# Kernel tuning notes

Hardware: AMD Instinct MI355X
Metric: run time of the kernel (lower is better)

## Reference

```python
import math
import jax, jax.numpy as jnp
import numpy as np

B, TQ, TK = 16, 2048, 1024
D_DEC, D_ENC, D_ATT = 256, 256, 128
WINDOW_SIZE = 3


def setup_inputs() -> dict:
    key = jax.random.key(0)
    ks = jax.random.split(key, 11)
    s = 0.02
    return {
        "query": jax.random.normal(ks[0], (B, TQ, D_DEC), jnp.float32),
        "keys": jax.random.normal(ks[1], (B, TK, D_ENC), jnp.float32),
        "values": jax.random.normal(ks[2], (B, TK, D_ENC), jnp.float32),
        "Wq": jax.random.normal(ks[3], (D_ATT, D_DEC), jnp.float32) * s,
        "bq": jax.random.normal(ks[4], (D_ATT,), jnp.float32) * s,
        "Wk": jax.random.normal(ks[5], (D_ATT, D_ENC), jnp.float32) * s,
        "bk": jax.random.normal(ks[6], (D_ATT,), jnp.float32) * s,
        "Wv": jax.random.normal(ks[7], (D_ATT, D_ENC), jnp.float32) * s,
        "bv": jax.random.normal(ks[8], (D_ATT,), jnp.float32) * s,
        "Wo": jax.random.normal(ks[9], (D_DEC, D_ATT), jnp.float32) * s,
        "bo": jax.random.normal(ks[10], (D_DEC,), jnp.float32) * s,
        "prev_max_attention_idx": 100,
    }


def reference(query, keys, values, Wq, bq, Wk, bk, Wv, bv, Wo, bo,
              prev_max_attention_idx):
    residual = query
    q = query @ Wq.T + bq            # [B, Tq, A]
    k = keys @ Wk.T + bk             # [B, Tk, A]
    v = values @ Wv.T + bv           # [B, Tk, A]
    scores = jnp.einsum('bqa,bka->bqk', q, k)  # [B, Tq, Tk]
    Tk = scores.shape[-1]
    col = jnp.arange(Tk)
    # mask [:prev] if prev > 0, and [prev + window :] if in range
    masked = (col < prev_max_attention_idx) | (col >= prev_max_attention_idx + WINDOW_SIZE)
    scores = jnp.where(masked[None, None, :], -jnp.inf, scores)
    attn = jax.nn.softmax(scores, axis=-1)
    attn_scores = attn
    # dropout_prob = 0.0 -> identity
    ctx = jnp.einsum('bqk,bka->bqa', attn, v)
    s = v.shape[1]
    ctx = ctx * (s * math.sqrt(1.0 / s))  # == sqrt(Tk)
    out = (ctx @ Wo.T + bo + residual) * math.sqrt(0.5)
    return (out, attn_scores)
```

## Files before the change

### kernel.cpp

```cpp
#include <hip/hip_runtime.h>
#include <math.h>

#define BATCH 16
#define TQL   2048
#define TKL   1024
#define DDEC  256
#define DENC  256
#define DATT  128
#define WIN   3

#define WS_KQ 0
#define WS_VO (48*DDEC)
#define WS_KB (2*48*DDEC)

__global__ __launch_bounds__(256) void precompute(
    const float* __restrict__ keys, const float* __restrict__ values,
    const float* __restrict__ Wk, const float* __restrict__ bk,
    const float* __restrict__ Wv, const float* __restrict__ bv,
    const float* __restrict__ Wq, const float* __restrict__ bq,
    const float* __restrict__ Wo, const int* __restrict__ pidx,
    float* __restrict__ ws)
{
    const int blk = blockIdx.x;
    const int b = blk / WIN, j = blk % WIN;
    const int prev = pidx[0];
    const int col = prev + j;
    const bool valid = (col >= 0) && (col < TKL);

    __shared__ float ksh[DENC];
    __shared__ float vsh[DENC];
    __shared__ float kwsh[DATT];
    __shared__ float vwsh[DATT];

    const int t = threadIdx.x;
    {
        size_t base = ((size_t)b * TKL + (valid ? col : 0)) * DENC + t;
        ksh[t] = valid ? keys[base]   : 0.0f;
        vsh[t] = valid ? values[base] : 0.0f;
    }
    __syncthreads();

    if (t < DATT) {
        const float4* wrow = (const float4*)(Wk + (size_t)t * DENC);
        float acc = 0.0f;
        #pragma unroll 8
        for (int k4 = 0; k4 < DENC / 4; ++k4) {
            float4 w = wrow[k4];
            acc += w.x * ksh[k4*4+0] + w.y * ksh[k4*4+1]
                 + w.z * ksh[k4*4+2] + w.w * ksh[k4*4+3];
        }
        kwsh[t] = acc + bk[t];
    } else {
        const int c = t - DATT;
        const float4* wrow = (const float4*)(Wv + (size_t)c * DENC);
        float acc = 0.0f;
        #pragma unroll 8
        for (int k4 = 0; k4 < DENC / 4; ++k4) {
            float4 w = wrow[k4];
            acc += w.x * vsh[k4*4+0] + w.y * vsh[k4*4+1]
                 + w.z * vsh[k4*4+2] + w.w * vsh[k4*4+3];
        }
        vwsh[c] = acc + bv[c];
    }
    __syncthreads();

    float accq = 0.0f, acco = 0.0f;
    const float4* worow = (const float4*)(Wo + (size_t)t * DATT);
    #pragma unroll 4
    for (int c4 = 0; c4 < DATT / 4; ++c4) {
        float4 w = worow[c4];
        acco += w.x * vwsh[c4*4+0] + w.y * vwsh[c4*4+1]
              + w.z * vwsh[c4*4+2] + w.w * vwsh[c4*4+3];
        accq += kwsh[c4*4+0] * Wq[(size_t)(c4*4+0) * DDEC + t]
              + kwsh[c4*4+1] * Wq[(size_t)(c4*4+1) * DDEC + t]
              + kwsh[c4*4+2] * Wq[(size_t)(c4*4+2) * DDEC + t]
              + kwsh[c4*4+3] * Wq[(size_t)(c4*4+3) * DDEC + t];
    }
    ws[WS_KQ + blk * DDEC + t] = accq;
    ws[WS_VO + blk * DDEC + t] = acco;

    if (t < 64) {
        float pb = bq[t] * kwsh[t] + bq[t + 64] * kwsh[t + 64];
        #pragma unroll
        for (int off = 32; off > 0; off >>= 1) pb += __shfl_xor(pb, off, 64);
        if (t == 0) ws[WS_KB + blk] = pb;
    }
}

__device__ __forceinline__ float winval(int ww, float w0, float w1, float w2) {
    float v = (ww == 0) ? w0 : ((ww == 1) ? w1 : ((ww == 2) ? w2 : 0.0f));
    return (ww >= 0 && ww < WIN) ? v : 0.0f;
}

__global__ __launch_bounds__(256) void attn_main(
    const float* __restrict__ query, const float* __restrict__ bo,
    const int* __restrict__ pidx, const float* __restrict__ ws,
    float* __restrict__ out, float* __restrict__ attn)
{
    const float* kq = ws + WS_KQ;
    const float* vo = ws + WS_VO;
    const float* kb = ws + WS_KB;
    const int prev = pidx[0];

    const int t    = threadIdx.x;
    const int lane = t & 63;
    const int wid  = t >> 6;
    const int g    = lane >> 4;
    const int sub  = lane & 15;
    const int row  = blockIdx.x * 16 + wid * 4 + g;
    const int b    = row >> 11;
    const int base = b * WIN;

    const float4* q4p = (const float4*)query + (size_t)row * 64;
    const float4 q0 = q4p[ 0 + sub];
    const float4 q1 = q4p[16 + sub];
    const float4 q2 = q4p[32 + sub];
    const float4 q3 = q4p[48 + sub];

    int lo = prev < 0 ? 0 : prev;
    int hi = prev + (WIN - 1) > TKL - 1 ? TKL - 1 : prev + (WIN - 1);
    int f0 = -1, f1 = -1;
    if (lo <= hi) { f0 = lo >> 2; f1 = hi >> 2; }

    float4* arow = (float4*)(attn + (size_t)row * TKL);
    const float4 z4 = make_float4(0.0f, 0.0f, 0.0f, 0.0f);
    #pragma unroll
    for (int s = 0; s < 16; ++s) {
        const int f = s * 16 + sub;
        if (f != f0 && f != f1) arow[f] = z4;
    }

    const float4* kqp0 = (const float4*)kq + (size_t)(base + 0) * 64;
    const float4* kqp1 = (const float4*)kq + (size_t)(base + 1) * 64;
    const float4* kqp2 = (const float4*)kq + (size_t)(base + 2) * 64;

    float p0, p1, p2;
    {
        float4 k0, k1, k2;
        k0 = kqp0[ 0 + sub]; k1 = kqp1[ 0 + sub]; k2 = kqp2[ 0 + sub];
        p0  = q0.x*k0.x + q0.y*k0.y + q0.z*k0.z + q0.w*k0.w;
        p1  = q0.x*k1.x + q0.y*k1.y + q0.z*k1.z + q0.w*k1.w;
        p2  = q0.x*k2.x + q0.y*k2.y + q0.z*k2.z + q0.w*k2.w;
        k0 = kqp0[16 + sub]; k1 = kqp1[16 + sub]; k2 = kqp2[16 + sub];
        p0 += q1.x*k0.x + q1.y*k0.y + q1.z*k0.z + q1.w*k0.w;
        p1 += q1.x*k1.x + q1.y*k1.y + q1.z*k1.z + q1.w*k1.w;
        p2 += q1.x*k2.x + q1.y*k2.y + q1.z*k2.z + q1.w*k2.w;
        k0 = kqp0[32 + sub]; k1 = kqp1[32 + sub]; k2 = kqp2[32 + sub];
        p0 += q2.x*k0.x + q2.y*k0.y + q2.z*k0.z + q2.w*k0.w;
        p1 += q2.x*k1.x + q2.y*k1.y + q2.z*k1.z + q2.w*k1.w;
        p2 += q2.x*k2.x + q2.y*k2.y + q2.z*k2.z + q2.w*k2.w;
        k0 = kqp0[48 + sub]; k1 = kqp1[48 + sub]; k2 = kqp2[48 + sub];
        p0 += q3.x*k0.x + q3.y*k0.y + q3.z*k0.z + q3.w*k0.w;
        p1 += q3.x*k1.x + q3.y*k1.y + q3.z*k1.z + q3.w*k1.w;
        p2 += q3.x*k2.x + q3.y*k2.y + q3.z*k2.z + q3.w*k2.w;
    }
    #pragma unroll
    for (int off = 8; off > 0; off >>= 1) {
        p0 += __shfl_xor(p0, off, 64);
        p1 += __shfl_xor(p1, off, 64);
        p2 += __shfl_xor(p2, off, 64);
    }

    float s0 = p0 + kb[base + 0];
    float s1 = p1 + kb[base + 1];
    float s2 = p2 + kb[base + 2];

    const bool v0 = (prev + 0 >= 0) && (prev + 0 < TKL);
    const bool v1 = (prev + 1 >= 0) && (prev + 1 < TKL);
    const bool v2 = (prev + 2 >= 0) && (prev + 2 < TKL);
    const float NEG = -3.0e38f;
    if (!v0) s0 = NEG;
    if (!v1) s1 = NEG;
    if (!v2) s2 = NEG;

    const float m  = fmaxf(s0, fmaxf(s1, s2));
    const float e0 = v0 ? __expf(s0 - m) : 0.0f;
    const float e1 = v1 ? __expf(s1 - m) : 0.0f;
    const float e2 = v2 ? __expf(s2 - m) : 0.0f;
    const float inv = 1.0f / (e0 + e1 + e2);
    const float w0 = e0 * inv, w1 = e1 * inv, w2 = e2 * inv;

    const float CTX_SCALE = 32.0f;
    const float RSQ2 = 0.70710678118654752f;

    const float4* vop0 = (const float4*)vo + (size_t)(base + 0) * 64;
    const float4* vop1 = (const float4*)vo + (size_t)(base + 1) * 64;
    const float4* vop2 = (const float4*)vo + (size_t)(base + 2) * 64;
    const float4* bo4p = (const float4*)bo;
    float4* orow = (float4*)(out + (size_t)row * DDEC);

    #pragma unroll
    for (int k = 0; k < 4; ++k) {
        const float4 x0 = vop0[k * 16 + sub];
        const float4 x1 = vop1[k * 16 + sub];
        const float4 x2 = vop2[k * 16 + sub];
        const float4 bb = bo4p[k * 16 + sub];
        const float4 qq = (k == 0) ? q0 : (k == 1) ? q1 : (k == 2) ? q2 : q3;
        float4 o;
        o.x = (CTX_SCALE * (w0*x0.x + w1*x1.x + w2*x2.x) + bb.x + qq.x) * RSQ2;
        o.y = (CTX_SCALE * (w0*x0.y + w1*x1.y + w2*x2.y) + bb.y + qq.y) * RSQ2;
        o.z = (CTX_SCALE * (w0*x0.z + w1*x1.z + w2*x2.z) + bb.z + qq.z) * RSQ2;
        o.w = (CTX_SCALE * (w0*x0.w + w1*x1.w + w2*x2.w) + bb.w + qq.w) * RSQ2;
        orow[k * 16 + sub] = o;
    }

    if (f0 >= 0 && (f0 & 15) == sub) {
        const int c0 = f0 * 4;
        float4 pz;
        pz.x = winval(c0 + 0 - prev, w0, w1, w2);
        pz.y = winval(c0 + 1 - prev, w0, w1, w2);
        pz.z = winval(c0 + 2 - prev, w0, w1, w2);
        pz.w = winval(c0 + 3 - prev, w0, w1, w2);
        arow[f0] = pz;
    }
    if (f1 >= 0 && f1 != f0 && (f1 & 15) == sub) {
        const int c0 = f1 * 4;
        float4 pz;
        pz.x = winval(c0 + 0 - prev, w0, w1, w2);
        pz.y = winval(c0 + 1 - prev, w0, w1, w2);
        pz.z = winval(c0 + 2 - prev, w0, w1, w2);
        pz.w = winval(c0 + 3 - prev, w0, w1, w2);
        arow[f1] = pz;
    }
}

extern "C" void kernel_launch(void* const* d_in, const int* in_sizes, int n_in,
                              void* d_out, int out_size, void* d_ws, size_t ws_size,
                              hipStream_t stream)
{
    const float* query  = (const float*)d_in[0];
    const float* keys   = (const float*)d_in[1];
    const float* values = (const float*)d_in[2];
    const float* Wq     = (const float*)d_in[3];
    const float* bq     = (const float*)d_in[4];
    const float* Wk     = (const float*)d_in[5];
    const float* bk     = (const float*)d_in[6];
    const float* Wv     = (const float*)d_in[7];
    const float* bv     = (const float*)d_in[8];
    const float* Wo     = (const float*)d_in[9];
    const float* bo     = (const float*)d_in[10];
    const int*   pidx   = (const int*)d_in[11];

    float* ws   = (float*)d_ws;
    float* out  = (float*)d_out;
    float* attn = out + (size_t)BATCH * TQL * DDEC;

    precompute<<<48, 256, 0, stream>>>(keys, values, Wk, bk, Wv, bv,
                                       Wq, bq, Wo, pidx, ws);
    attn_main<<<BATCH * TQL / 16, 256, 0, stream>>>(query, bo, pidx, ws, out, attn);
}
```

Before: 50.07 us.

## Move attention-matrix zero fill into precompute kernel as extra blocks

```diff
diff --git a/kernel.cpp b/kernel.cpp
--- a/kernel.cpp
+++ b/kernel.cpp
@@ -13,14 +13,27 @@
 #define WS_VO (48*DDEC)
 #define WS_KB (2*48*DDEC)
 
-__global__ __launch_bounds__(256) void precompute(
+#define NZBLK 2048
+
+__global__ __launch_bounds__(256) void pre_and_zero(
     const float* __restrict__ keys, const float* __restrict__ values,
     const float* __restrict__ Wk, const float* __restrict__ bk,
     const float* __restrict__ Wv, const float* __restrict__ bv,
     const float* __restrict__ Wq, const float* __restrict__ bq,
     const float* __restrict__ Wo, const int* __restrict__ pidx,
-    float* __restrict__ ws)
+    float* __restrict__ ws, float* __restrict__ attn)
 {
+    const int t = threadIdx.x;
+
+    if (blockIdx.x >= 48) {
+        const int zb = blockIdx.x - 48;
+        float4* p = (float4*)attn + (size_t)zb * 4096;
+        const float4 z4 = make_float4(0.0f, 0.0f, 0.0f, 0.0f);
+        #pragma unroll
+        for (int i = 0; i < 16; ++i) p[i * 256 + t] = z4;
+        return;
+    }
+
     const int blk = blockIdx.x;
     const int b = blk / WIN, j = blk % WIN;
     const int prev = pidx[0];
@@ -32,7 +45,6 @@
     __shared__ float kwsh[DATT];
     __shared__ float vwsh[DATT];
 
-    const int t = threadIdx.x;
     {
         size_t base = ((size_t)b * TKL + (valid ? col : 0)) * DENC + t;
         ksh[t] = valid ? keys[base]   : 0.0f;
@@ -92,7 +104,7 @@
     return (ww >= 0 && ww < WIN) ? v : 0.0f;
 }
 
-__global__ __launch_bounds__(256) void attn_main(
+__global__ __launch_bounds__(256) void attn_out(
     const float* __restrict__ query, const float* __restrict__ bo,
     const int* __restrict__ pidx, const float* __restrict__ ws,
     float* __restrict__ out, float* __restrict__ attn)
@@ -116,19 +128,6 @@
     const float4 q1 = q4p[16 + sub];
     const float4 q2 = q4p[32 + sub];
     const float4 q3 = q4p[48 + sub];
-
-    int lo = prev < 0 ? 0 : prev;
-    int hi = prev + (WIN - 1) > TKL - 1 ? TKL - 1 : prev + (WIN - 1);
-    int f0 = -1, f1 = -1;
-    if (lo <= hi) { f0 = lo >> 2; f1 = hi >> 2; }
-
-    float4* arow = (float4*)(attn + (size_t)row * TKL);
-    const float4 z4 = make_float4(0.0f, 0.0f, 0.0f, 0.0f);
-    #pragma unroll
-    for (int s = 0; s < 16; ++s) {
-        const int f = s * 16 + sub;
-        if (f != f0 && f != f1) arow[f] = z4;
-    }
 
     const float4* kqp0 = (const float4*)kq + (size_t)(base + 0) * 64;
     const float4* kqp1 = (const float4*)kq + (size_t)(base + 1) * 64;
@@ -204,23 +203,29 @@
         orow[k * 16 + sub] = o;
     }
 
-    if (f0 >= 0 && (f0 & 15) == sub) {
-        const int c0 = f0 * 4;
-        float4 pz;
-        pz.x = winval(c0 + 0 - prev, w0, w1, w2);
-        pz.y = winval(c0 + 1 - prev, w0, w1, w2);
-        pz.z = winval(c0 + 2 - prev, w0, w1, w2);
-        pz.w = winval(c0 + 3 - prev, w0, w1, w2);
-        arow[f0] = pz;
-    }
-    if (f1 >= 0 && f1 != f0 && (f1 & 15) == sub) {
-        const int c0 = f1 * 4;
-        float4 pz;
-        pz.x = winval(c0 + 0 - prev, w0, w1, w2);
-        pz.y = winval(c0 + 1 - prev, w0, w1, w2);
-        pz.z = winval(c0 + 2 - prev, w0, w1, w2);
-        pz.w = winval(c0 + 3 - prev, w0, w1, w2);
-        arow[f1] = pz;
+    int lo = prev < 0 ? 0 : prev;
+    int hi = prev + (WIN - 1) > TKL - 1 ? TKL - 1 : prev + (WIN - 1);
+    if (lo <= hi) {
+        const int f0 = lo >> 2, f1 = hi >> 2;
+        float4* arow = (float4*)(attn + (size_t)row * TKL);
+        if ((f0 & 15) == sub) {
+            const int c0 = f0 * 4;
+            float4 pz;
+            pz.x = winval(c0 + 0 - prev, w0, w1, w2);
+            pz.y = winval(c0 + 1 - prev, w0, w1, w2);
+            pz.z = winval(c0 + 2 - prev, w0, w1, w2);
+            pz.w = winval(c0 + 3 - prev, w0, w1, w2);
+            arow[f0] = pz;
+        }
+        if (f1 != f0 && (f1 & 15) == sub) {
+            const int c0 = f1 * 4;
+            float4 pz;
+            pz.x = winval(c0 + 0 - prev, w0, w1, w2);
+            pz.y = winval(c0 + 1 - prev, w0, w1, w2);
+            pz.z = winval(c0 + 2 - prev, w0, w1, w2);
+            pz.w = winval(c0 + 3 - prev, w0, w1, w2);
+            arow[f1] = pz;
+        }
     }
 }
 
@@ -245,7 +250,7 @@
     float* out  = (float*)d_out;
     float* attn = out + (size_t)BATCH * TQL * DDEC;
 
-    precompute<<<48, 256, 0, stream>>>(keys, values, Wk, bk, Wv, bv,
-                                       Wq, bq, Wo, pidx, ws);
-    attn_main<<<BATCH * TQL / 16, 256, 0, stream>>>(query, bo, pidx, ws, out, attn);
-}
+    pre_and_zero<<<48 + NZBLK, 256, 0, stream>>>(keys, values, Wk, bk, Wv, bv,
+                                                 Wq, bq, Wo, pidx, ws, attn);
+    attn_out<<<BATCH * TQL / 16, 256, 0, stream>>>(query, bo, pidx, ws, out, attn);
+}
```

Result: faster. 41.95 us (-16.2%).
